# Kernel tuning notes

Measured on AMD Instinct MI355X. Metric: run time of the kernel, lower is better.

## Reference

```python
import jax, jax.numpy as jnp
import numpy as np

BATCH, SENT = 4096, 8192

def setup_inputs() -> dict:
    key = jax.random.key(0)
    k1, k2, k3 = jax.random.split(key, 3)
    # keep pred strictly inside (0,1) so log terms are finite
    pred = jax.random.uniform(k1, (BATCH, SENT), dtype=jnp.float32, minval=0.01, maxval=0.99)
    labels = jax.random.randint(k2, (BATCH, SENT), 0, 2, dtype=jnp.int32)
    weight = jax.random.uniform(k3, (BATCH,), dtype=jnp.float32)
    return {"pred": pred, "labels": labels, "weight": weight}

def reference(pred, labels, weight):
    # elementwise weighted BCE:
    #   label == 0 -> -log(1 - pred)
    #   label == 1 -> -weight[i] * log(pred)
    neg = -jnp.log1p(-pred)                      # [B, S]
    pos = -(weight[:, None] * jnp.log(pred))      # [B, S]
    return jnp.where(labels == 0, neg, pos)       # [B, S]
```

## Files before the change

### kernel.cpp

```cpp
#include <hip/hip_runtime.h>


#define WBCE_BATCH 4096
#define WBCE_SENT  8192
#define LOG2_VEC_PER_ROW 11

__global__ __launch_bounds__(256) void WeightedBCELoss_70128226009669_kernel(
    const float4* __restrict__ pred4,
    const int4*  __restrict__ lab4,
    const float* __restrict__ weight,
    float4* __restrict__ out4)
{
    const int i = blockIdx.x * 256 + threadIdx.x;
    const int row = i >> LOG2_VEC_PER_ROW;
    const float w = weight[row];

    const float4 p = pred4[i];
    const int4  l = lab4[i];

    const float x0 = (l.x == 0) ? (1.0f - p.x) : p.x;
    const float x1 = (l.y == 0) ? (1.0f - p.y) : p.y;
    const float x2 = (l.z == 0) ? (1.0f - p.z) : p.z;
    const float x3 = (l.w == 0) ? (1.0f - p.w) : p.w;

    const float s0 = (l.x == 0) ? 1.0f : w;
    const float s1 = (l.y == 0) ? 1.0f : w;
    const float s2 = (l.z == 0) ? 1.0f : w;
    const float s3 = (l.w == 0) ? 1.0f : w;

    float4 o;
    o.x = -s0 * __logf(x0);
    o.y = -s1 * __logf(x1);
    o.z = -s2 * __logf(x2);
    o.w = -s3 * __logf(x3);

    out4[i] = o;
}

extern "C" void kernel_launch(void* const* d_in, const int* in_sizes, int n_in,
                              void* d_out, int out_size, void* d_ws, size_t ws_size,
                              hipStream_t stream) {
    const float4* pred4  = (const float4*)d_in[0];
    const int4*   lab4   = (const int4*)d_in[1];
    const float*  weight = (const float*)d_in[2];
    float4* out4 = (float4*)d_out;

    const int n_vec = (WBCE_BATCH * WBCE_SENT) / 4;
    const int block = 256;
    const int grid = n_vec / block;

    WeightedBCELoss_70128226009669_kernel<<<grid, block, 0, stream>>>(
        pred4, lab4, weight, out4);
}
```

Before: 302.1 us.

## Use grid-stride loop with batched vector loads and nontemporal stores

Replaces the one-vector-per-thread launch with a fixed grid where each thread loops over strided chunks, issuing four float4/int4 load pairs before computing so more memory requests are in flight. Outputs are written with nontemporal stores to avoid polluting caches. The row weight is made wave-uniform via readfirstlane, and the natural log is computed as log2 times a folded -ln2 scale. Fewer blocks means less launch/scheduling overhead but relies on enough waves per CU to saturate bandwidth.

New measurement: 331.6 us. 1.1x slower.

```diff
diff --git a/kernel.cpp b/kernel.cpp
--- a/kernel.cpp
+++ b/kernel.cpp
@@ -4,37 +4,63 @@
 #define WBCE_BATCH 4096
 #define WBCE_SENT  8192
 #define LOG2_VEC_PER_ROW 11
+#define N_VEC   (WBCE_BATCH * (WBCE_SENT / 4))
 
-__global__ __launch_bounds__(256) void WeightedBCELoss_70128226009669_kernel(
+#define THREADS 256
+#define BLOCKS  2048
+#define STRIDE  (BLOCKS * THREADS)
+#define ITERS   (N_VEC / STRIDE)
+#define BATCHN  4
+
+typedef float f32x4 __attribute__((ext_vector_type(4)));
+
+__global__ __launch_bounds__(THREADS) void WeightedBCELoss_70128226009669_kernel(
     const float4* __restrict__ pred4,
     const int4*  __restrict__ lab4,
     const float* __restrict__ weight,
     float4* __restrict__ out4)
 {
-    const int i = blockIdx.x * 256 + threadIdx.x;
-    const int row = i >> LOG2_VEC_PER_ROW;
-    const float w = weight[row];
+    const int tid = blockIdx.x * THREADS + threadIdx.x;
+    constexpr float NEG_LN2 = -0.69314718055994530942f;
 
-    const float4 p = pred4[i];
-    const int4  l = lab4[i];
+    for (int u = 0; u < ITERS; u += BATCHN) {
+        float4 p[BATCHN];
+        int4   l[BATCHN];
 
-    const float x0 = (l.x == 0) ? (1.0f - p.x) : p.x;
-    const float x1 = (l.y == 0) ? (1.0f - p.y) : p.y;
-    const float x2 = (l.z == 0) ? (1.0f - p.z) : p.z;
-    const float x3 = (l.w == 0) ? (1.0f - p.w) : p.w;
+        const int base = tid + u * STRIDE;
 
-    const float s0 = (l.x == 0) ? 1.0f : w;
-    const float s1 = (l.y == 0) ? 1.0f : w;
-    const float s2 = (l.z == 0) ? 1.0f : w;
-    const float s3 = (l.w == 0) ? 1.0f : w;
+        #pragma unroll
+        for (int k = 0; k < BATCHN; ++k) {
+            p[k] = pred4[base + k * STRIDE];
+            l[k] = lab4[base + k * STRIDE];
+        }
 
-    float4 o;
-    o.x = -s0 * __logf(x0);
-    o.y = -s1 * __logf(x1);
-    o.z = -s2 * __logf(x2);
-    o.w = -s3 * __logf(x3);
+        #pragma unroll
+        for (int k = 0; k < BATCHN; ++k) {
+            const int idx = base + k * STRIDE;
 
-    out4[i] = o;
+            const int row = __builtin_amdgcn_readfirstlane(idx >> LOG2_VEC_PER_ROW);
+            const float wn = weight[row] * NEG_LN2;
+
+            const float x0 = (l[k].x == 0) ? (1.0f - p[k].x) : p[k].x;
+            const float x1 = (l[k].y == 0) ? (1.0f - p[k].y) : p[k].y;
+            const float x2 = (l[k].z == 0) ? (1.0f - p[k].z) : p[k].z;
+            const float x3 = (l[k].w == 0) ? (1.0f - p[k].w) : p[k].w;
+
+            const float s0 = (l[k].x == 0) ? NEG_LN2 : wn;
+            const float s1 = (l[k].y == 0) ? NEG_LN2 : wn;
+            const float s2 = (l[k].z == 0) ? NEG_LN2 : wn;
+            const float s3 = (l[k].w == 0) ? NEG_LN2 : wn;
+
+            f32x4 o;
+            o.x = s0 * __log2f(x0);
+            o.y = s1 * __log2f(x1);
+            o.z = s2 * __log2f(x2);
+            o.w = s3 * __log2f(x3);
+
+            __builtin_nontemporal_store(o, (f32x4*)&out4[idx]);
+        }
+    }
 }
 
 extern "C" void kernel_launch(void* const* d_in, const int* in_sizes, int n_in,
@@ -45,10 +71,6 @@
     const float*  weight = (const float*)d_in[2];
     float4* out4 = (float4*)d_out;
 
-    const int n_vec = (WBCE_BATCH * WBCE_SENT) / 4;
-    const int block = 256;
-    const int grid = n_vec / block;
-
-    WeightedBCELoss_70128226009669_kernel<<<grid, block, 0, stream>>>(
+    WeightedBCELoss_70128226009669_kernel<<<BLOCKS, THREADS, 0, stream>>>(
         pred4, lab4, weight, out4);
 }
```
